# Kernel tuning notes

Hardware: AMD Instinct MI355X
Metric: run time of the kernel (lower is better)

## Reference

```python
import jax, jax.numpy as jnp
import numpy as np

def setup_inputs() -> dict:
    key = jax.random.key(0)
    k1, k2, k3, k4, k5 = jax.random.split(key, 5)
    H = 1024
    B, T = 32, 1024
    hidden = jax.random.normal(k1, (1, B, H), dtype=jnp.float32)
    encoder_outputs = jax.random.normal(k2, (B, T, H), dtype=jnp.float32)
    # nn.Linear(2H, H): weight [H, 2H], bias [H]
    bound = 1.0 / np.sqrt(2 * H)
    W = jax.random.uniform(k3, (H, 2 * H), minval=-bound, maxval=bound, dtype=jnp.float32)
    b = jax.random.uniform(k4, (H,), minval=-bound, maxval=bound, dtype=jnp.float32)
    v = jax.random.uniform(k5, (H,), dtype=jnp.float32)  # torch.rand
    return {"hidden": hidden, "encoder_outputs": encoder_outputs, "W": W, "b": b, "v": v}

def reference(hidden, encoder_outputs, W, b, v):
    B = hidden.shape[1]
    H = hidden.shape[2]
    h = jnp.transpose(hidden, (1, 0, 2)).reshape(B, -1)  # [B, H]
    # Split Linear(2H->H): cat([h_rep, enc]) @ W.T == h @ Wh.T + enc @ We.T
    Wh, We = W[:, :H], W[:, H:]
    # [B,1,H] + [B,T,H] -> [B,T,H]
    pre = jnp.tanh((h @ Wh.T + b)[:, None, :] + jnp.einsum('bth,gh->btg', encoder_outputs, We))
    energies = jnp.einsum('bth,h->bt', pre, v)  # [B, T]
    return jax.nn.softmax(energies, axis=1)[:, None, :]  # [B, 1, T]
```

## Files before the change

kernel.cpp:

```cpp
#include <hip/hip_runtime.h>
#include <hip/hip_fp16.h>

typedef _Float16 half8  __attribute__((ext_vector_type(8)));
typedef _Float16 half4_t __attribute__((ext_vector_type(4)));
typedef float    f32x4  __attribute__((ext_vector_type(4)));

#define HDIM  1024
#define BATCH 32
#define TLEN  1024
#define M_TOT (BATCH * TLEN)

#define BM 128
#define BN 128
#define BK 32
#define LDA 40

__global__ void zero_k(float* __restrict__ p) {
    p[blockIdx.x * blockDim.x + threadIdx.x] = 0.f;
}

__global__ void we_convert_k(const float* __restrict__ W, _Float16* __restrict__ We16) {
    int idx = blockIdx.x * blockDim.x + threadIdx.x;
    int g  = idx >> 8;
    int k4 = idx & 255;
    float4 f = *reinterpret_cast<const float4*>(W + (size_t)g * 2048 + 1024 + k4 * 4);
    half4_t h;
    h[0] = (_Float16)f.x; h[1] = (_Float16)f.y; h[2] = (_Float16)f.z; h[3] = (_Float16)f.w;
    *reinterpret_cast<half4_t*>(We16 + (size_t)idx * 4) = h;
}

__global__ void qproj_k(const float* __restrict__ hidden, const float* __restrict__ W,
                        const float* __restrict__ bias, float* __restrict__ q) {
    int g = blockIdx.x;
    int t = threadIdx.x;
    int wave = t >> 6, lane = t & 63;
    float acc[BATCH];
#pragma unroll
    for (int b = 0; b < BATCH; b++) acc[b] = 0.f;
    const float* wr = W + (size_t)g * 2048;
    for (int h = t; h < HDIM; h += 256) {
        float w = wr[h];
#pragma unroll
        for (int b = 0; b < BATCH; b++) acc[b] = fmaf(w, hidden[b * HDIM + h], acc[b]);
    }
    __shared__ float sm[4 * BATCH];
#pragma unroll
    for (int b = 0; b < BATCH; b++) {
        float s = acc[b];
#pragma unroll
        for (int off = 32; off >= 1; off >>= 1) s += __shfl_xor(s, off);
        if (lane == 0) sm[wave * BATCH + b] = s;
    }
    __syncthreads();
    if (t < BATCH) {
        float s = sm[t] + sm[BATCH + t] + sm[2 * BATCH + t] + sm[3 * BATCH + t];
        q[t * HDIM + g] = s + bias[g];
    }
}

__global__ __launch_bounds__(256, 2)
void attn_gemm_k(const float* __restrict__ enc, const _Float16* __restrict__ We16,
                 const float* __restrict__ q, const float* __restrict__ v,
                 float* __restrict__ energies) {
    __shared__ _Float16 As[BM * LDA];
    __shared__ _Float16 Bs[BN * LDA];

    const int tid  = threadIdx.x;
    const int n0   = blockIdx.x * BN;
    const int m0   = blockIdx.y * BM;
    const int wave = tid >> 6;
    const int lane = tid & 63;
    const int quad = lane >> 4;
    const int l16  = lane & 15;
    const int wm   = (wave & 1) * 64;
    const int wn   = (wave >> 1) * 64;

    const int srow = tid >> 1;
    const int scol = (tid & 1) * 16;

    f32x4 acc[4][4];
#pragma unroll
    for (int i = 0; i < 4; i++)
#pragma unroll
        for (int j = 0; j < 4; j++) acc[i][j] = {0.f, 0.f, 0.f, 0.f};

    const float*    ag = enc  + (size_t)(m0 + srow) * HDIM + scol;
    const _Float16* bg = We16 + (size_t)(n0 + srow) * HDIM + scol;
    _Float16* aw = &As[srow * LDA + scol];
    _Float16* bw = &Bs[srow * LDA + scol];

    for (int k0 = 0; k0 < HDIM; k0 += BK) {
        float4 a0 = *reinterpret_cast<const float4*>(ag + k0 + 0);
        float4 a1 = *reinterpret_cast<const float4*>(ag + k0 + 4);
        float4 a2 = *reinterpret_cast<const float4*>(ag + k0 + 8);
        float4 a3 = *reinterpret_cast<const float4*>(ag + k0 + 12);
        float4 b0 = *reinterpret_cast<const float4*>(bg + k0);
        float4 b1 = *reinterpret_cast<const float4*>(bg + k0 + 8);

        __syncthreads();

        half8 ha0, ha1;
        ha0[0] = (_Float16)a0.x; ha0[1] = (_Float16)a0.y; ha0[2] = (_Float16)a0.z; ha0[3] = (_Float16)a0.w;
        ha0[4] = (_Float16)a1.x; ha0[5] = (_Float16)a1.y; ha0[6] = (_Float16)a1.z; ha0[7] = (_Float16)a1.w;
        ha1[0] = (_Float16)a2.x; ha1[1] = (_Float16)a2.y; ha1[2] = (_Float16)a2.z; ha1[3] = (_Float16)a2.w;
        ha1[4] = (_Float16)a3.x; ha1[5] = (_Float16)a3.y; ha1[6] = (_Float16)a3.z; ha1[7] = (_Float16)a3.w;
        *reinterpret_cast<half8*>(aw)     = ha0;
        *reinterpret_cast<half8*>(aw + 8) = ha1;
        *reinterpret_cast<float4*>(bw)     = b0;
        *reinterpret_cast<float4*>(bw + 8) = b1;

        __syncthreads();

        half8 af[4], bf[4];
#pragma unroll
        for (int i = 0; i < 4; i++) {
            af[i] = *reinterpret_cast<const half8*>(&As[(wm + i * 16 + l16) * LDA + quad * 8]);
            bf[i] = *reinterpret_cast<const half8*>(&Bs[(wn + i * 16 + l16) * LDA + quad * 8]);
        }
#pragma unroll
        for (int mi = 0; mi < 4; mi++)
#pragma unroll
            for (int ni = 0; ni < 4; ni++)
                acc[mi][ni] = __builtin_amdgcn_mfma_f32_16x16x32_f16(af[mi], bf[ni], acc[mi][ni], 0, 0, 0);
    }

    const int bidx = m0 >> 10;
    float qv[4], vv[4];
#pragma unroll
    for (int ni = 0; ni < 4; ni++) {
        int g = n0 + wn + ni * 16 + l16;
        qv[ni] = q[bidx * HDIM + g];
        vv[ni] = v[g];
    }
#pragma unroll
    for (int mi = 0; mi < 4; mi++) {
#pragma unroll
        for (int r = 0; r < 4; r++) {
            int row = wm + mi * 16 + quad * 4 + r;
            float s = 0.f;
#pragma unroll
            for (int ni = 0; ni < 4; ni++) {
                float pre = acc[mi][ni][r] + qv[ni];
                float e = __expf(2.f * pre);
                float th = 1.f - 2.f / (e + 1.f);
                s = fmaf(th, vv[ni], s);
            }
            s += __shfl_xor(s, 1);
            s += __shfl_xor(s, 2);
            s += __shfl_xor(s, 4);
            s += __shfl_xor(s, 8);
            if (l16 == 0) atomicAdd(&energies[m0 + row], s);
        }
    }
}

__global__ void softmax_k(const float* __restrict__ energies, float* __restrict__ out) {
    int b = blockIdx.x;
    int t = threadIdx.x;
    int wave = t >> 6, lane = t & 63;
    __shared__ float smax[4], ssum[4];
    float e[4];
#pragma unroll
    for (int i = 0; i < 4; i++) e[i] = energies[b * TLEN + t + i * 256];
    float m = fmaxf(fmaxf(e[0], e[1]), fmaxf(e[2], e[3]));
#pragma unroll
    for (int off = 32; off >= 1; off >>= 1) m = fmaxf(m, __shfl_xor(m, off));
    if (lane == 0) smax[wave] = m;
    __syncthreads();
    float M = fmaxf(fmaxf(smax[0], smax[1]), fmaxf(smax[2], smax[3]));
    float x[4]; float s = 0.f;
#pragma unroll
    for (int i = 0; i < 4; i++) { x[i] = __expf(e[i] - M); s += x[i]; }
#pragma unroll
    for (int off = 32; off >= 1; off >>= 1) s += __shfl_xor(s, off);
    if (lane == 0) ssum[wave] = s;
    __syncthreads();
    float S = ssum[0] + ssum[1] + ssum[2] + ssum[3];
    float inv = 1.f / S;
#pragma unroll
    for (int i = 0; i < 4; i++) out[b * TLEN + t + i * 256] = x[i] * inv;
}

extern "C" void kernel_launch(void* const* d_in, const int* in_sizes, int n_in,
                              void* d_out, int out_size, void* d_ws, size_t ws_size,
                              hipStream_t stream) {
    const float* hidden = (const float*)d_in[0];
    const float* enc    = (const float*)d_in[1];
    const float* W      = (const float*)d_in[2];
    const float* bias   = (const float*)d_in[3];
    const float* v      = (const float*)d_in[4];
    float* out = (float*)d_out;

    char* ws = (char*)d_ws;
    float*    q     = (float*)ws;
    float*    energ = (float*)(ws + 131072);
    _Float16* We16  = (_Float16*)(ws + 262144);

    zero_k<<<dim3(M_TOT / 256), 256, 0, stream>>>(energ);
    we_convert_k<<<dim3(1024), 256, 0, stream>>>(W, We16);
    qproj_k<<<dim3(HDIM), 256, 0, stream>>>(hidden, W, bias, q);
    attn_gemm_k<<<dim3(8, 256), 256, 0, stream>>>(enc, We16, q, v, energ);
    softmax_k<<<dim3(BATCH), 256, 0, stream>>>(energ, out);
}
```

Before: 341.2 us.

## Pre-convert encoder outputs to fp16 and stream GEMM tiles via direct global-to-LDS loads

Adds a pass that converts the fp32 encoder outputs to fp16 in the workspace. A new GEMM kernel then loads both operand tiles with 16-byte global_load_lds async copies, so the per-tile register round trip and the fp32-to-fp16 conversion no longer sit in the inner loop. The grid is also reordered so the M tile index runs along blockIdx.x, which changes L2 reuse of encoder rows. The cost is an extra full read/write pass over the encoder tensor, an unpadded LDS layout that may cause bank conflicts, and a dependence on having enough workspace, with the old kernel kept as a fallback.

Result: faster. 324.7 us (-4.8%).

```diff
diff --git a/kernel.cpp b/kernel.cpp
--- a/kernel.cpp
+++ b/kernel.cpp
@@ -1,9 +1,9 @@
 #include <hip/hip_runtime.h>
 #include <hip/hip_fp16.h>
 
-typedef _Float16 half8  __attribute__((ext_vector_type(8)));
+typedef _Float16 half8   __attribute__((ext_vector_type(8)));
 typedef _Float16 half4_t __attribute__((ext_vector_type(4)));
-typedef float    f32x4  __attribute__((ext_vector_type(4)));
+typedef float    f32x4   __attribute__((ext_vector_type(4)));
 
 #define HDIM  1024
 #define BATCH 32
@@ -29,6 +29,16 @@
     *reinterpret_cast<half4_t*>(We16 + (size_t)idx * 4) = h;
 }
 
+__global__ void enc_convert_k(const float* __restrict__ enc, _Float16* __restrict__ enc16) {
+    size_t i = ((size_t)blockIdx.x * blockDim.x + threadIdx.x) * 8;
+    float4 f0 = *reinterpret_cast<const float4*>(enc + i);
+    float4 f1 = *reinterpret_cast<const float4*>(enc + i + 4);
+    half8 h;
+    h[0] = (_Float16)f0.x; h[1] = (_Float16)f0.y; h[2] = (_Float16)f0.z; h[3] = (_Float16)f0.w;
+    h[4] = (_Float16)f1.x; h[5] = (_Float16)f1.y; h[6] = (_Float16)f1.z; h[7] = (_Float16)f1.w;
+    *reinterpret_cast<half8*>(enc16 + i) = h;
+}
+
 __global__ void qproj_k(const float* __restrict__ hidden, const float* __restrict__ W,
                         const float* __restrict__ bias, float* __restrict__ q) {
     int g = blockIdx.x;
@@ -58,16 +68,22 @@
     }
 }
 
-__global__ __launch_bounds__(256, 2)
-void attn_gemm_k(const float* __restrict__ enc, const _Float16* __restrict__ We16,
-                 const float* __restrict__ q, const float* __restrict__ v,
-                 float* __restrict__ energies) {
-    __shared__ _Float16 As[BM * LDA];
-    __shared__ _Float16 Bs[BN * LDA];
+__device__ __forceinline__ void async16(const void* g, void* l) {
+    __builtin_amdgcn_global_load_lds(
+        (const __attribute__((address_space(1))) void*)g,
+        (__attribute__((address_space(3))) void*)l, 16, 0, 0);
+}
+
+__global__ void attn_gemm_lds_k(const _Float16* __restrict__ enc16,
+                                const _Float16* __restrict__ We16,
+                                const float* __restrict__ q, const float* __restrict__ v,
+                                float* __restrict__ energies) {
+    __shared__ _Float16 As[BM * BK];
+    __shared__ _Float16 Bs[BN * BK];
 
     const int tid  = threadIdx.x;
-    const int n0   = blockIdx.x * BN;
-    const int m0   = blockIdx.y * BM;
+    const int m0   = blockIdx.x * BM;
+    const int n0   = blockIdx.y * BN;
     const int wave = tid >> 6;
     const int lane = tid & 63;
     const int quad = lane >> 4;
@@ -75,47 +91,33 @@
     const int wm   = (wave & 1) * 64;
     const int wn   = (wave >> 1) * 64;
 
-    const int srow = tid >> 1;
-    const int scol = (tid & 1) * 16;
-
     f32x4 acc[4][4];
 #pragma unroll
     for (int i = 0; i < 4; i++)
 #pragma unroll
         for (int j = 0; j < 4; j++) acc[i][j] = {0.f, 0.f, 0.f, 0.f};
 
-    const float*    ag = enc  + (size_t)(m0 + srow) * HDIM + scol;
-    const _Float16* bg = We16 + (size_t)(n0 + srow) * HDIM + scol;
-    _Float16* aw = &As[srow * LDA + scol];
-    _Float16* bw = &Bs[srow * LDA + scol];
+    const int arow = wave * 16 + (lane >> 2);
+    const int acol = (lane & 3) * 8;
+    const _Float16* gA = enc16 + (size_t)(m0 + arow) * HDIM + acol;
+    const _Float16* gB = We16  + (size_t)(n0 + arow) * HDIM + acol;
+    _Float16* lA = As + wave * 512;
+    _Float16* lB = Bs + wave * 512;
+    const size_t gstep = (size_t)64 * HDIM;
 
     for (int k0 = 0; k0 < HDIM; k0 += BK) {
-        float4 a0 = *reinterpret_cast<const float4*>(ag + k0 + 0);
-        float4 a1 = *reinterpret_cast<const float4*>(ag + k0 + 4);
-        float4 a2 = *reinterpret_cast<const float4*>(ag + k0 + 8);
-        float4 a3 = *reinterpret_cast<const float4*>(ag + k0 + 12);
-        float4 b0 = *reinterpret_cast<const float4*>(bg + k0);
-        float4 b1 = *reinterpret_cast<const float4*>(bg + k0 + 8);
-
         __syncthreads();
-
-        half8 ha0, ha1;
-        ha0[0] = (_Float16)a0.x; ha0[1] = (_Float16)a0.y; ha0[2] = (_Float16)a0.z; ha0[3] = (_Float16)a0.w;
-        ha0[4] = (_Float16)a1.x; ha0[5] = (_Float16)a1.y; ha0[6] = (_Float16)a1.z; ha0[7] = (_Float16)a1.w;
-        ha1[0] = (_Float16)a2.x; ha1[1] = (_Float16)a2.y; ha1[2] = (_Float16)a2.z; ha1[3] = (_Float16)a2.w;
-        ha1[4] = (_Float16)a3.x; ha1[5] = (_Float16)a3.y; ha1[6] = (_Float16)a3.z; ha1[7] = (_Float16)a3.w;
-        *reinterpret_cast<half8*>(aw)     = ha0;
-        *reinterpret_cast<half8*>(aw + 8) = ha1;
-        *reinterpret_cast<float4*>(bw)     = b0;
-        *reinterpret_cast<float4*>(bw + 8) = b1;
-
+        async16(gA + k0, lA);
+        async16(gA + k0 + gstep, lA + 2048);
+        async16(gB + k0, lB);
+        async16(gB + k0 + gstep, lB + 2048);
         __syncthreads();
 
         half8 af[4], bf[4];
 #pragma unroll
         for (int i = 0; i < 4; i++) {
-            af[i] = *reinterpret_cast<const half8*>(&As[(wm + i * 16 + l16) * LDA + quad * 8]);
-            bf[i] = *reinterpret_cast<const half8*>(&Bs[(wn + i * 16 + l16) * LDA + quad * 8]);
+            af[i] = *reinterpret_cast<const half8*>(&As[(wm + i * 16 + l16) * BK + quad * 8]);
+            bf[i] = *reinterpret_cast<const half8*>(&Bs[(wn + i * 16 + l16) * BK + quad * 8]);
         }
 #pragma unroll
         for (int mi = 0; mi < 4; mi++)
@@ -154,6 +156,102 @@
     }
 }
 
+__global__ __launch_bounds__(256, 2)
+void attn_gemm_k(const float* __restrict__ enc, const _Float16* __restrict__ We16,
+                 const float* __restrict__ q, const float* __restrict__ v,
+                 float* __restrict__ energies) {
+    __shared__ _Float16 As[BM * LDA];
+    __shared__ _Float16 Bs[BN * LDA];
+
+    const int tid  = threadIdx.x;
+    const int m0   = blockIdx.x * BM;
+    const int n0   = blockIdx.y * BN;
+    const int wave = tid >> 6;
+    const int lane = tid & 63;
+    const int quad = lane >> 4;
+    const int l16  = lane & 15;
+    const int wm   = (wave & 1) * 64;
+    const int wn   = (wave >> 1) * 64;
+
+    const int srow = tid >> 1;
+    const int scol = (tid & 1) * 16;
+
+    f32x4 acc[4][4];
+#pragma unroll
+    for (int i = 0; i < 4; i++)
+#pragma unroll
+        for (int j = 0; j < 4; j++) acc[i][j] = {0.f, 0.f, 0.f, 0.f};
+
+    const float*    ag = enc  + (size_t)(m0 + srow) * HDIM + scol;
+    const _Float16* bg = We16 + (size_t)(n0 + srow) * HDIM + scol;
+    _Float16* aw = &As[srow * LDA + scol];
+    _Float16* bw = &Bs[srow * LDA + scol];
+
+    for (int k0 = 0; k0 < HDIM; k0 += BK) {
+        float4 a0 = *reinterpret_cast<const float4*>(ag + k0 + 0);
+        float4 a1 = *reinterpret_cast<const float4*>(ag + k0 + 4);
+        float4 a2 = *reinterpret_cast<const float4*>(ag + k0 + 8);
+        float4 a3 = *reinterpret_cast<const float4*>(ag + k0 + 12);
+        float4 b0 = *reinterpret_cast<const float4*>(bg + k0);
+        float4 b1 = *reinterpret_cast<const float4*>(bg + k0 + 8);
+
+        __syncthreads();
+
+        half8 ha0, ha1;
+        ha0[0] = (_Float16)a0.x; ha0[1] = (_Float16)a0.y; ha0[2] = (_Float16)a0.z; ha0[3] = (_Float16)a0.w;
+        ha0[4] = (_Float16)a1.x; ha0[5] = (_Float16)a1.y; ha0[6] = (_Float16)a1.z; ha0[7] = (_Float16)a1.w;
+        ha1[0] = (_Float16)a2.x; ha1[1] = (_Float16)a2.y; ha1[2] = (_Float16)a2.z; ha1[3] = (_Float16)a2.w;
+        ha1[4] = (_Float16)a3.x; ha1[5] = (_Float16)a3.y; ha1[6] = (_Float16)a3.z; ha1[7] = (_Float16)a3.w;
+        *reinterpret_cast<half8*>(aw)     = ha0;
+        *reinterpret_cast<half8*>(aw + 8) = ha1;
+        *reinterpret_cast<float4*>(bw)     = b0;
+        *reinterpret_cast<float4*>(bw + 8) = b1;
+
+        __syncthreads();
+
+        half8 af[4], bf[4];
+#pragma unroll
+        for (int i = 0; i < 4; i++) {
+            af[i] = *reinterpret_cast<const half8*>(&As[(wm + i * 16 + l16) * LDA + quad * 8]);
+            bf[i] = *reinterpret_cast<const half8*>(&Bs[(wn + i * 16 + l16) * LDA + quad * 8]);
+        }
+#pragma unroll
+        for (int mi = 0; mi < 4; mi++)
+#pragma unroll
+            for (int ni = 0; ni < 4; ni++)
+                acc[mi][ni] = __builtin_amdgcn_mfma_f32_16x16x32_f16(af[mi], bf[ni], acc[mi][ni], 0, 0, 0);
+    }
+
+    const int bidx = m0 >> 10;
+    float qv[4], vv[4];
+#pragma unroll
+    for (int ni = 0; ni < 4; ni++) {
+        int g = n0 + wn + ni * 16 + l16;
+        qv[ni] = q[bidx * HDIM + g];
+        vv[ni] = v[g];
+    }
+#pragma unroll
+    for (int mi = 0; mi < 4; mi++) {
+#pragma unroll
+        for (int r = 0; r < 4; r++) {
+            int row = wm + mi * 16 + quad * 4 + r;
+            float s = 0.f;
+#pragma unroll
+            for (int ni = 0; ni < 4; ni++) {
+                float pre = acc[mi][ni][r] + qv[ni];
+                float e = __expf(2.f * pre);
+                float th = 1.f - 2.f / (e + 1.f);
+                s = fmaf(th, vv[ni], s);
+            }
+            s += __shfl_xor(s, 1);
+            s += __shfl_xor(s, 2);
+            s += __shfl_xor(s, 4);
+            s += __shfl_xor(s, 8);
+            if (l16 == 0) atomicAdd(&energies[m0 + row], s);
+        }
+    }
+}
+
 __global__ void softmax_k(const float* __restrict__ energies, float* __restrict__ out) {
     int b = blockIdx.x;
     int t = threadIdx.x;
@@ -195,10 +293,17 @@
     float*    q     = (float*)ws;
     float*    energ = (float*)(ws + 131072);
     _Float16* We16  = (_Float16*)(ws + 262144);
+    _Float16* enc16 = (_Float16*)(ws + 262144 + 2097152);
+    const size_t need_fast = 262144 + 2097152 + (size_t)M_TOT * HDIM * 2;
 
     zero_k<<<dim3(M_TOT / 256), 256, 0, stream>>>(energ);
     we_convert_k<<<dim3(1024), 256, 0, stream>>>(W, We16);
     qproj_k<<<dim3(HDIM), 256, 0, stream>>>(hidden, W, bias, q);
-    attn_gemm_k<<<dim3(8, 256), 256, 0, stream>>>(enc, We16, q, v, energ);
+    if (ws_size >= need_fast) {
+        enc_convert_k<<<dim3((size_t)M_TOT * HDIM / 8 / 256), 256, 0, stream>>>(enc, enc16);
+        attn_gemm_lds_k<<<dim3(256, 8), 256, 0, stream>>>(enc16, We16, q, v, energ);
+    } else {
+        attn_gemm_k<<<dim3(256, 8), 256, 0, stream>>>(enc, We16, q, v, energ);
+    }
     softmax_k<<<dim3(BATCH), 256, 0, stream>>>(energ, out);
 }
```

## Pipeline GEMM with async LDS loads, swizzled tiles, XCD-aware mapping, merged prep kernels

Applied to the files above, without the earlier changes.

Merges the zeroing, weight conversion and query projection into one prep launch. The attention GEMM now uses BK=64 with XOR-swizzled LDS tiles instead of padding. The next B tile is fetched straight into LDS with global_load_lds, and the next fp32 A tile is prefetched into registers while the MFMAs run. Blocks are remapped so that tiles sharing the same encoder rows land on the same XCD, which is meant to improve L2 reuse. This cuts launch overhead and exposed load latency, at the cost of more registers and a single LDS buffer that relies on barrier ordering.

New measurement: 415.4 us. 21.7% more time.

```diff
diff --git a/kernel.cpp b/kernel.cpp
--- a/kernel.cpp
+++ b/kernel.cpp
@@ -1,9 +1,9 @@
 #include <hip/hip_runtime.h>
 #include <hip/hip_fp16.h>
 
-typedef _Float16 half8  __attribute__((ext_vector_type(8)));
+typedef _Float16 half8   __attribute__((ext_vector_type(8)));
 typedef _Float16 half4_t __attribute__((ext_vector_type(4)));
-typedef float    f32x4  __attribute__((ext_vector_type(4)));
+typedef float    f32x4   __attribute__((ext_vector_type(4)));
 
 #define HDIM  1024
 #define BATCH 32
@@ -12,62 +12,72 @@
 
 #define BM 128
 #define BN 128
-#define BK 32
-#define LDA 40
-
-__global__ void zero_k(float* __restrict__ p) {
-    p[blockIdx.x * blockDim.x + threadIdx.x] = 0.f;
-}
-
-__global__ void we_convert_k(const float* __restrict__ W, _Float16* __restrict__ We16) {
-    int idx = blockIdx.x * blockDim.x + threadIdx.x;
-    int g  = idx >> 8;
-    int k4 = idx & 255;
-    float4 f = *reinterpret_cast<const float4*>(W + (size_t)g * 2048 + 1024 + k4 * 4);
-    half4_t h;
-    h[0] = (_Float16)f.x; h[1] = (_Float16)f.y; h[2] = (_Float16)f.z; h[3] = (_Float16)f.w;
-    *reinterpret_cast<half4_t*>(We16 + (size_t)idx * 4) = h;
-}
-
-__global__ void qproj_k(const float* __restrict__ hidden, const float* __restrict__ W,
-                        const float* __restrict__ bias, float* __restrict__ q) {
-    int g = blockIdx.x;
-    int t = threadIdx.x;
-    int wave = t >> 6, lane = t & 63;
-    float acc[BATCH];
-#pragma unroll
-    for (int b = 0; b < BATCH; b++) acc[b] = 0.f;
-    const float* wr = W + (size_t)g * 2048;
-    for (int h = t; h < HDIM; h += 256) {
-        float w = wr[h];
-#pragma unroll
-        for (int b = 0; b < BATCH; b++) acc[b] = fmaf(w, hidden[b * HDIM + h], acc[b]);
-    }
-    __shared__ float sm[4 * BATCH];
-#pragma unroll
-    for (int b = 0; b < BATCH; b++) {
-        float s = acc[b];
-#pragma unroll
-        for (int off = 32; off >= 1; off >>= 1) s += __shfl_xor(s, off);
-        if (lane == 0) sm[wave * BATCH + b] = s;
-    }
-    __syncthreads();
-    if (t < BATCH) {
-        float s = sm[t] + sm[BATCH + t] + sm[2 * BATCH + t] + sm[3 * BATCH + t];
-        q[t * HDIM + g] = s + bias[g];
-    }
-}
-
-__global__ __launch_bounds__(256, 2)
-void attn_gemm_k(const float* __restrict__ enc, const _Float16* __restrict__ We16,
-                 const float* __restrict__ q, const float* __restrict__ v,
-                 float* __restrict__ energies) {
-    __shared__ _Float16 As[BM * LDA];
-    __shared__ _Float16 Bs[BN * LDA];
+#define BK 64
+#define NIT (HDIM / BK)
+
+__global__ void prep_k(const float* __restrict__ W, const float* __restrict__ hidden,
+                       const float* __restrict__ bias, _Float16* __restrict__ We16,
+                       float* __restrict__ q, float* __restrict__ energ) {
+    const int bid = blockIdx.x;
+    const int t = threadIdx.x;
+    if (bid < 1024) {
+        int idx = bid * 256 + t;
+        int g  = idx >> 8;
+        int k4 = idx & 255;
+        float4 f = *reinterpret_cast<const float4*>(W + (size_t)g * 2048 + 1024 + k4 * 4);
+        half4_t h;
+        h[0] = (_Float16)f.x; h[1] = (_Float16)f.y; h[2] = (_Float16)f.z; h[3] = (_Float16)f.w;
+        *reinterpret_cast<half4_t*>(We16 + (size_t)idx * 4) = h;
+    } else if (bid < 2048) {
+        int g = bid - 1024;
+        int wave = t >> 6, lane = t & 63;
+        float acc[BATCH];
+#pragma unroll
+        for (int b = 0; b < BATCH; b++) acc[b] = 0.f;
+        const float* wr = W + (size_t)g * 2048;
+        for (int h = t; h < HDIM; h += 256) {
+            float w = wr[h];
+#pragma unroll
+            for (int b = 0; b < BATCH; b++) acc[b] = fmaf(w, hidden[b * HDIM + h], acc[b]);
+        }
+        __shared__ float sm[4 * BATCH];
+#pragma unroll
+        for (int b = 0; b < BATCH; b++) {
+            float s = acc[b];
+#pragma unroll
+            for (int off = 32; off >= 1; off >>= 1) s += __shfl_xor(s, off);
+            if (lane == 0) sm[wave * BATCH + b] = s;
+        }
+        __syncthreads();
+        if (t < BATCH) {
+            float s = sm[t] + sm[BATCH + t] + sm[2 * BATCH + t] + sm[3 * BATCH + t];
+            q[t * HDIM + g] = s + bias[g];
+        }
+    } else {
+        energ[(bid - 2048) * 256 + t] = 0.f;
+    }
+}
+
+__device__ __forceinline__ void async16(const void* g, void* l) {
+    __builtin_amdgcn_global_load_lds(
+        (const __attribute__((address_space(1))) void*)g,
+        (__attribute__((address_space(3))) void*)l, 16, 0, 0);
+}
+
+__global__ __launch_bounds__(256)
+void attn_gemm_fused_k(const float* __restrict__ enc,
+                       const _Float16* __restrict__ We16,
+                       const float* __restrict__ q, const float* __restrict__ v,
+                       float* __restrict__ energies) {
+    __shared__ _Float16 As[BM * BK];
+    __shared__ _Float16 Bs[BN * BK];
 
     const int tid  = threadIdx.x;
-    const int n0   = blockIdx.x * BN;
-    const int m0   = blockIdx.y * BM;
+    const int id   = blockIdx.x;
+    const int xcd  = id & 7;
+    const int w    = id >> 3;
+    const int m0   = (xcd * 32 + (w >> 3)) * BM;
+    const int n0   = (w & 7) * BN;
     const int wave = tid >> 6;
     const int lane = tid & 63;
     const int quad = lane >> 4;
@@ -75,53 +85,94 @@
     const int wm   = (wave & 1) * 64;
     const int wn   = (wave >> 1) * 64;
 
-    const int srow = tid >> 1;
-    const int scol = (tid & 1) * 16;
-
     f32x4 acc[4][4];
 #pragma unroll
     for (int i = 0; i < 4; i++)
 #pragma unroll
         for (int j = 0; j < 4; j++) acc[i][j] = {0.f, 0.f, 0.f, 0.f};
 
-    const float*    ag = enc  + (size_t)(m0 + srow) * HDIM + scol;
-    const _Float16* bg = We16 + (size_t)(n0 + srow) * HDIM + scol;
-    _Float16* aw = &As[srow * LDA + scol];
-    _Float16* bw = &Bs[srow * LDA + scol];
-
-    for (int k0 = 0; k0 < HDIM; k0 += BK) {
-        float4 a0 = *reinterpret_cast<const float4*>(ag + k0 + 0);
-        float4 a1 = *reinterpret_cast<const float4*>(ag + k0 + 4);
-        float4 a2 = *reinterpret_cast<const float4*>(ag + k0 + 8);
-        float4 a3 = *reinterpret_cast<const float4*>(ag + k0 + 12);
-        float4 b0 = *reinterpret_cast<const float4*>(bg + k0);
-        float4 b1 = *reinterpret_cast<const float4*>(bg + k0 + 8);
-
+    const int arow = tid >> 1;
+    const int ahalf = tid & 1;
+    const float* gA = enc + (size_t)(m0 + arow) * HDIM + ahalf * 32;
+    const int aswz = arow & 7;
+    const int abase = arow * BK;
+
+    const int bsrow = wave * 32 + (lane >> 3);
+    const int bscol = ((lane & 7) ^ (lane >> 3)) * 8;
+    const _Float16* gB = We16 + (size_t)(n0 + bsrow) * HDIM + bscol;
+    _Float16* lB = Bs + wave * 2048;
+    const size_t bistep = (size_t)8 * HDIM;
+
+#pragma unroll
+    for (int ii = 0; ii < 4; ii++) async16(gB + ii * bistep, lB + ii * 512);
+    {
+        float4 fl[8];
+#pragma unroll
+        for (int j = 0; j < 8; j++) fl[j] = *reinterpret_cast<const float4*>(gA + j * 4);
+#pragma unroll
+        for (int j = 0; j < 4; j++) {
+            half8 h;
+            h[0] = (_Float16)fl[2*j].x;   h[1] = (_Float16)fl[2*j].y;
+            h[2] = (_Float16)fl[2*j].z;   h[3] = (_Float16)fl[2*j].w;
+            h[4] = (_Float16)fl[2*j+1].x; h[5] = (_Float16)fl[2*j+1].y;
+            h[6] = (_Float16)fl[2*j+1].z; h[7] = (_Float16)fl[2*j+1].w;
+            *reinterpret_cast<half8*>(&As[abase + (((4*ahalf + j) ^ aswz) * 8)]) = h;
+        }
+    }
+    __syncthreads();
+
+    int aoff[2][4], boff[2][4];
+#pragma unroll
+    for (int s = 0; s < 2; s++)
+#pragma unroll
+        for (int i = 0; i < 4; i++) {
+            int ra = wm + i * 16 + l16;
+            int rb = wn + i * 16 + l16;
+            aoff[s][i] = ra * BK + (((s * 4 + quad) ^ (l16 & 7)) * 8);
+            boff[s][i] = rb * BK + (((s * 4 + quad) ^ (l16 & 7)) * 8);
+        }
+
+    for (int it = 0; it < NIT; it++) {
+        half8 af[2][4], bf[2][4];
+#pragma unroll
+        for (int s = 0; s < 2; s++)
+#pragma unroll
+            for (int i = 0; i < 4; i++) {
+                af[s][i] = *reinterpret_cast<const half8*>(&As[aoff[s][i]]);
+                bf[s][i] = *reinterpret_cast<const half8*>(&Bs[boff[s][i]]);
+            }
         __syncthreads();
 
-        half8 ha0, ha1;
-        ha0[0] = (_Float16)a0.x; ha0[1] = (_Float16)a0.y; ha0[2] = (_Float16)a0.z; ha0[3] = (_Float16)a0.w;
-        ha0[4] = (_Float16)a1.x; ha0[5] = (_Float16)a1.y; ha0[6] = (_Float16)a1.z; ha0[7] = (_Float16)a1.w;
-        ha1[0] = (_Float16)a2.x; ha1[1] = (_Float16)a2.y; ha1[2] = (_Float16)a2.z; ha1[3] = (_Float16)a2.w;
-        ha1[4] = (_Float16)a3.x; ha1[5] = (_Float16)a3.y; ha1[6] = (_Float16)a3.z; ha1[7] = (_Float16)a3.w;
-        *reinterpret_cast<half8*>(aw)     = ha0;
-        *reinterpret_cast<half8*>(aw + 8) = ha1;
-        *reinterpret_cast<float4*>(bw)     = b0;
-        *reinterpret_cast<float4*>(bw + 8) = b1;
-
+        float4 fl[8];
+        const bool more = (it + 1 < NIT);
+        if (more) {
+            const int k = (it + 1) * BK;
+#pragma unroll
+            for (int ii = 0; ii < 4; ii++) async16(gB + k + ii * bistep, lB + ii * 512);
+#pragma unroll
+            for (int j = 0; j < 8; j++) fl[j] = *reinterpret_cast<const float4*>(gA + k + j * 4);
+        }
+
+#pragma unroll
+        for (int s = 0; s < 2; s++)
+#pragma unroll
+            for (int mi = 0; mi < 4; mi++)
+#pragma unroll
+                for (int ni = 0; ni < 4; ni++)
+                    acc[mi][ni] = __builtin_amdgcn_mfma_f32_16x16x32_f16(af[s][mi], bf[s][ni], acc[mi][ni], 0, 0, 0);
+
+        if (more) {
+#pragma unroll
+            for (int j = 0; j < 4; j++) {
+                half8 h;
+                h[0] = (_Float16)fl[2*j].x;   h[1] = (_Float16)fl[2*j].y;
+                h[2] = (_Float16)fl[2*j].z;   h[3] = (_Float16)fl[2*j].w;
+                h[4] = (_Float16)fl[2*j+1].x; h[5] = (_Float16)fl[2*j+1].y;
+                h[6] = (_Float16)fl[2*j+1].z; h[7] = (_Float16)fl[2*j+1].w;
+                *reinterpret_cast<half8*>(&As[abase + (((4*ahalf + j) ^ aswz) * 8)]) = h;
+            }
+        }
         __syncthreads();
-
-        half8 af[4], bf[4];
-#pragma unroll
-        for (int i = 0; i < 4; i++) {
-            af[i] = *reinterpret_cast<const half8*>(&As[(wm + i * 16 + l16) * LDA + quad * 8]);
-            bf[i] = *reinterpret_cast<const half8*>(&Bs[(wn + i * 16 + l16) * LDA + quad * 8]);
-        }
-#pragma unroll
-        for (int mi = 0; mi < 4; mi++)
-#pragma unroll
-            for (int ni = 0; ni < 4; ni++)
-                acc[mi][ni] = __builtin_amdgcn_mfma_f32_16x16x32_f16(af[mi], bf[ni], acc[mi][ni], 0, 0, 0);
     }
 
     const int bidx = m0 >> 10;
@@ -196,9 +247,7 @@
     float*    energ = (float*)(ws + 131072);
     _Float16* We16  = (_Float16*)(ws + 262144);
 
-    zero_k<<<dim3(M_TOT / 256), 256, 0, stream>>>(energ);
-    we_convert_k<<<dim3(1024), 256, 0, stream>>>(W, We16);
-    qproj_k<<<dim3(HDIM), 256, 0, stream>>>(hidden, W, bias, q);
-    attn_gemm_k<<<dim3(8, 256), 256, 0, stream>>>(enc, We16, q, v, energ);
+    prep_k<<<dim3(2176), 256, 0, stream>>>(W, hidden, bias, We16, q, energ);
+    attn_gemm_fused_k<<<dim3(2048), 256, 0, stream>>>(enc, We16, q, v, energ);
     softmax_k<<<dim3(BATCH), 256, 0, stream>>>(energ, out);
 }
```
